# Kernel optimization log

Measured on AMD Instinct MI355X. Metric: run time of the kernel, lower is better.

The kernel has to match this reference:

```python
import jax
import jax.numpy as jnp
import numpy as np
from jax import lax

# Grid / problem dimensions (match init_kwargs / input_specs)
B = 1          # batch_size
D, H, W = 16, 128, 128   # full-resolution voxel grid (z, y, x)
N = 120000     # number of occupied voxels
CIN = 16       # num_input_features
EPS = 1e-5     # MinkowskiBatchNorm eps (eval mode, running stats)


def setup_inputs() -> dict:
    key = jax.random.key(0)
    ks = jax.random.split(key, 24)

    # Unique voxel coordinates (ME.SparseTensor coordinates are unique after quantization)
    perm = jax.random.permutation(ks[0], D * H * W)[:N]
    z = (perm // (H * W)).astype(jnp.int32)
    y = ((perm // W) % H).astype(jnp.int32)
    x = (perm % W).astype(jnp.int32)
    coors = jnp.stack([jnp.zeros(N, jnp.int32), z, y, x], axis=1)  # (batch, z, y, x)

    voxel_features = jax.random.normal(ks[1], (N, CIN), jnp.float32)

    def w(k, shape, fan_in):
        return jax.random.normal(k, shape, jnp.float32) * (1.0 / np.sqrt(fan_in))

    w0 = w(ks[2], (32, 16, 3, 3, 3), 16 * 27)
    w1 = w(ks[3], (32, 32, 3, 3, 3), 32 * 27)
    w2 = w(ks[4], (64, 32, 3, 3, 3), 32 * 27)
    w64 = w(ks[5], (7, 64, 64, 3, 3, 3), 64 * 27)   # the seven 64->64 k=3^3 convs
    w10 = w(ks[6], (64, 64, 3, 1, 1), 64 * 3)        # final k=(3,1,1) conv

    bn32_gamma = 1.0 + 0.1 * jax.random.normal(ks[7], (2, 32), jnp.float32)
    bn32_beta = 0.1 * jax.random.normal(ks[8], (2, 32), jnp.float32)
    bn32_mean = 0.1 * jax.random.normal(ks[9], (2, 32), jnp.float32)
    bn32_var = 0.5 + jax.random.uniform(ks[10], (2, 32), jnp.float32)
    bn64_gamma = 1.0 + 0.1 * jax.random.normal(ks[11], (9, 64), jnp.float32)
    bn64_beta = 0.1 * jax.random.normal(ks[12], (9, 64), jnp.float32)
    bn64_mean = 0.1 * jax.random.normal(ks[13], (9, 64), jnp.float32)
    bn64_var = 0.5 + jax.random.uniform(ks[14], (9, 64), jnp.float32)

    return {
        "voxel_features": voxel_features, "coors": coors,
        "w0": w0, "w1": w1, "w2": w2, "w64": w64, "w10": w10,
        "bn32_gamma": bn32_gamma, "bn32_beta": bn32_beta,
        "bn32_mean": bn32_mean, "bn32_var": bn32_var,
        "bn64_gamma": bn64_gamma, "bn64_beta": bn64_beta,
        "bn64_mean": bn64_mean, "bn64_var": bn64_var,
        "batch_size": B,
    }


def _conv(x, w, stride_z):
    # Minkowski conv with odd kernel is a centered conv; in the z-downsampled
    # dense grid, kernel offsets scaled by tensor stride reduce to ordinary
    # dense conv with 'half' padding per axis and stride on z.
    pads = [(w.shape[2] // 2,) * 2, (w.shape[3] // 2,) * 2, (w.shape[4] // 2,) * 2]
    return lax.conv_general_dilated(
        x, w, (stride_z, 1, 1), pads,
        dimension_numbers=("NCDHW", "OIDHW", "NCDHW"))


def _bn_relu(x, g, b, m, v):
    inv = g / jnp.sqrt(v + EPS)                    # [C]
    sh = (1, -1, 1, 1, 1)
    return jax.nn.relu(x * inv.reshape(sh) + (b - m * inv).reshape(sh))


def _pool_z(occ):
    # strided Minkowski conv output coords = unique(floor(c/2)) of input coords
    return jnp.maximum(occ[:, :, 0::2], occ[:, :, 1::2])


def reference(voxel_features, coors, w0, w1, w2, w64, w10,
              bn32_gamma, bn32_beta, bn32_mean, bn32_var,
              bn64_gamma, bn64_beta, bn64_mean, bn64_var, batch_size):
    b, z, y, x = coors[:, 0], coors[:, 1], coors[:, 2], coors[:, 3]
    # Densify sparse tensor (unoccupied voxels are exact zeros, as in ME)
    h = jnp.zeros((batch_size, D, H, W, CIN), voxel_features.dtype)
    h = h.at[b, z, y, x].set(voxel_features)
    h = jnp.moveaxis(h, -1, 1)                                   # [B,C,D,H,W]
    occ = jnp.zeros((batch_size, 1, D, H, W), voxel_features.dtype)
    occ = occ.at[b, 0, z, y, x].set(1.0)

    # Two 32-channel stride-1 convs: output coords == input coords -> mask with occ
    h = _bn_relu(_conv(h, w0, 1), bn32_gamma[0], bn32_beta[0], bn32_mean[0], bn32_var[0]) * occ
    h = _bn_relu(_conv(h, w1, 1), bn32_gamma[1], bn32_beta[1], bn32_mean[1], bn32_var[1]) * occ

    # 32->64, stride (2,1,1)
    occ = _pool_z(occ)
    h = _bn_relu(_conv(h, w2, 2), bn64_gamma[0], bn64_beta[0], bn64_mean[0], bn64_var[0]) * occ
    # three 64->64 stride-1 convs
    for i in range(3):
        h = _bn_relu(_conv(h, w64[i], 1), bn64_gamma[1 + i], bn64_beta[1 + i], bn64_mean[1 + i], bn64_var[1 + i]) * occ
    # 64->64 stride (2,1,1)
    occ = _pool_z(occ)
    h = _bn_relu(_conv(h, w64[3], 2), bn64_gamma[4], bn64_beta[4], bn64_mean[4], bn64_var[4]) * occ
    # three 64->64 stride-1 convs
    for i in range(3):
        h = _bn_relu(_conv(h, w64[4 + i], 1), bn64_gamma[5 + i], bn64_beta[5 + i], bn64_mean[5 + i], bn64_var[5 + i]) * occ
    # final 64->64, kernel (3,1,1), stride (2,1,1)
    occ = _pool_z(occ)
    h = _bn_relu(_conv(h, w10, 2), bn64_gamma[8], bn64_beta[8], bn64_mean[8], bn64_var[8]) * occ

    # prune is a no-op (all coords in-range by construction); dense() -> [B,C,Dz,H,W]
    n, c, d, hh, ww = h.shape
    return h.reshape(n, c * d, hh, ww)
```

## Files before the change

kernel.cpp:

```cpp
#include <hip/hip_runtime.h>

#define HW 16384

typedef _Float16 half8  __attribute__((ext_vector_type(8)));
typedef _Float16 half4v __attribute__((ext_vector_type(4)));
typedef float    f32x4  __attribute__((ext_vector_type(4)));

typedef __attribute__((address_space(3))) unsigned int lds_u32;
typedef const __attribute__((address_space(1))) unsigned int glb_u32;

__device__ __forceinline__ void gl_lds16(const void* g, void* l) {
    __builtin_amdgcn_global_load_lds((glb_u32*)g, (lds_u32*)l, 16, 0, 0);
}

__global__ void zero4(float4* __restrict__ p, int n4) {
    int i = blockIdx.x * 256 + threadIdx.x;
    if (i < n4) p[i] = make_float4(0.f, 0.f, 0.f, 0.f);
}

__global__ void write_code_f32(float* out, float v) {
    if (threadIdx.x == 0 && blockIdx.x == 0) out[0] = v;
}

__global__ void pack_w(const float* __restrict__ W, _Float16* __restrict__ dst,
                       int CINr, int CINp, int COUT, int KD, int KHW, int NSTEPS) {
    int idx = blockIdx.x * 256 + threadIdx.x;
    int total = (COUT / 16) * NSTEPS * 64;
    if (idx >= total) return;
    int lane = idx & 63;
    int s    = (idx >> 6) % NSTEPS;
    int grp  = idx / (NSTEPS * 64);
    int k0  = s * 32 + (lane >> 4) * 8;
    int t   = k0 / CINp;
    int ci0 = k0 % CINp;
    int co  = grp * 16 + (lane & 15);
    int khw2 = KHW * KHW;
    int dz = t / khw2, r = t % khw2, dy = r / KHW, dx = r % KHW;
    half8 hv;
    for (int j = 0; j < 8; ++j) {
        int ci = ci0 + j;
        float wv = (ci < CINr)
            ? W[(((size_t)co * CINr + ci) * KD + dz) * khw2 + dy * KHW + dx] : 0.0f;
        hv[j] = (_Float16)wv;
    }
    *(half8*)(dst + ((size_t)(grp * NSTEPS + s) * 64 + lane) * 8) = hv;
}

__global__ void scatter_f16(const float* __restrict__ vf, const int* __restrict__ coors,
                            _Float16* __restrict__ act, unsigned char* __restrict__ occ, int n) {
    int i = blockIdx.x * 256 + threadIdx.x;
    if (i >= n) return;
    int z = coors[i * 4 + 1];
    int y = coors[i * 4 + 2];
    int x = coors[i * 4 + 3];
    size_t cell = ((size_t)(z * 130 + (y + 1)) * 130 + (x + 1)) * 40;
    for (int c = 0; c < 16; ++c) act[cell + c] = (_Float16)vf[i * 16 + c];
    occ[z * HW + y * 128 + x] = 1;
}

__global__ void pool_occ(const unsigned char* __restrict__ o0, unsigned char* __restrict__ o1,
                         unsigned char* __restrict__ o2, unsigned char* __restrict__ o3) {
    int p = blockIdx.x * 256 + threadIdx.x;
    if (p >= HW) return;
    unsigned char a[16];
    for (int z = 0; z < 16; ++z) a[z] = o0[z * HW + p];
    for (int z = 0; z < 8; ++z) { a[z] = a[2 * z] | a[2 * z + 1]; o1[z * HW + p] = a[z]; }
    for (int z = 0; z < 4; ++z) { a[z] = a[2 * z] | a[2 * z + 1]; o2[z * HW + p] = a[z]; }
    for (int z = 0; z < 2; ++z) { a[z] = a[2 * z] | a[2 * z + 1]; o3[z * HW + p] = a[z]; }
}

template <int CINp, int COUT, int KD, int KHW, int SZ, int DIN, int DOUT, bool FINAL>
__global__ __launch_bounds__(256, 2)
void conv_mfma(const _Float16* __restrict__ act, const _Float16* __restrict__ apack,
               const float* __restrict__ gm, const float* __restrict__ bt,
               const float* __restrict__ mn, const float* __restrict__ vr,
               const unsigned char* __restrict__ occ, void* __restrict__ outv) {
    constexpr int PADXY  = KHW / 2;
    constexpr int CB     = CINp / 32;
    constexpr int MG     = COUT / 16;
    constexpr int NSTEPS = KD * KHW * KHW * CB;
    constexpr int CS     = CINp + 8;
    constexpr int OCS    = COUT + 8;
    constexpr int NGRAN  = 4 * 130 * CS / 8;
    constexpr int NIT    = (NGRAN + 255) / 256;
    constexpr int OFS    = 1 - PADXY;

    __shared__ _Float16 smem[4 * 130 * CS];

    const int bid = blockIdx.x;
    const int yp = bid & 63;
    const int z0 = bid >> 6;
    const int y0 = yp * 2;
    const int tid  = threadIdx.x;
    const int w    = tid >> 6;
    const int lane = tid & 63;
    const int ylocal = w >> 1;
    const int x0w    = (w & 1) * 64;
    const int n  = lane & 15;
    const int kg = lane >> 4;

    f32x4 acc[MG][4];
    #pragma unroll
    for (int m = 0; m < MG; ++m)
        #pragma unroll
        for (int t = 0; t < 4; ++t) { acc[m][t][0] = 0.f; acc[m][t][1] = 0.f; acc[m][t][2] = 0.f; acc[m][t][3] = 0.f; }

    const int zb = z0 * SZ;
    const int dzlo = (zb == 0) ? 1 : 0;
    const int dzhi = (zb + KD - 1 > DIN) ? (KD - 1) : KD;

    for (int dz = dzlo; dz < dzhi; ++dz) {
        const int zi = zb + dz - 1;
        __syncthreads();
        const _Float16* src = act + (size_t)(zi * 130 + y0) * (130 * CS);
        #pragma unroll
        for (int it = 0; it < NIT; ++it) {
            int g = it * 256 + tid;
            if (g < NGRAN) gl_lds16(src + (size_t)g * 8, smem + (size_t)g * 8);
        }
        asm volatile("s_waitcnt vmcnt(0)" ::: "memory");
        __syncthreads();
        #pragma unroll
        for (int dy = 0; dy < KHW; ++dy) {
            #pragma unroll
            for (int dx = 0; dx < KHW; ++dx) {
                #pragma unroll
                for (int cb = 0; cb < CB; ++cb) {
                    const int sabs = dz * (KHW * KHW * CB) + (dy * KHW + dx) * CB + cb;
                    half8 a[MG];
                    #pragma unroll
                    for (int mg = 0; mg < MG; ++mg)
                        a[mg] = *(const half8*)(apack + ((size_t)(mg * NSTEPS + sabs) * 64 + lane) * 8);
                    const _Float16* bp = smem
                        + ((ylocal + dy + OFS) * 130 + x0w + n + dx + OFS) * CS + cb * 32 + kg * 8;
                    #pragma unroll
                    for (int nt = 0; nt < 4; ++nt) {
                        half8 b = *(const half8*)(bp + nt * 16 * CS);
                        #pragma unroll
                        for (int mg = 0; mg < MG; ++mg)
                            acc[mg][nt] = __builtin_amdgcn_mfma_f32_16x16x32_f16(a[mg], b, acc[mg][nt], 0, 0, 0);
                    }
                }
            }
        }
    }

    const int yo = y0 + ylocal;
    #pragma unroll
    for (int mg = 0; mg < MG; ++mg) {
        const int co0 = mg * 16 + kg * 4;
        const f32x4 gv = *(const f32x4*)(gm + co0);
        const f32x4 bv = *(const f32x4*)(bt + co0);
        const f32x4 mv = *(const f32x4*)(mn + co0);
        const f32x4 vv = *(const f32x4*)(vr + co0);
        float sc[4], sh[4];
        #pragma unroll
        for (int r = 0; r < 4; ++r) {
            sc[r] = gv[r] * __frsqrt_rn(vv[r] + 1e-5f);
            sh[r] = bv[r] - mv[r] * sc[r];
        }
        #pragma unroll
        for (int nt = 0; nt < 4; ++nt) {
            const int x = x0w + nt * 16 + n;
            const float occv = (float)occ[z0 * HW + yo * 128 + x];
            float v0 = fmaxf(fmaf(acc[mg][nt][0], sc[0], sh[0]), 0.f) * occv;
            float v1 = fmaxf(fmaf(acc[mg][nt][1], sc[1], sh[1]), 0.f) * occv;
            float v2 = fmaxf(fmaf(acc[mg][nt][2], sc[2], sh[2]), 0.f) * occv;
            float v3 = fmaxf(fmaf(acc[mg][nt][3], sc[3], sh[3]), 0.f) * occv;
            if constexpr (FINAL) {
                float* o = (float*)outv;
                const int sp = yo * 128 + x;
                o[((size_t)(co0 + 0) * 2 + z0) * HW + sp] = v0;
                o[((size_t)(co0 + 1) * 2 + z0) * HW + sp] = v1;
                o[((size_t)(co0 + 2) * 2 + z0) * HW + sp] = v2;
                o[((size_t)(co0 + 3) * 2 + z0) * HW + sp] = v3;
            } else {
                _Float16* o = (_Float16*)outv;
                half4v hv;
                hv[0] = (_Float16)v0; hv[1] = (_Float16)v1;
                hv[2] = (_Float16)v2; hv[3] = (_Float16)v3;
                *(half4v*)(o + ((size_t)(z0 * 130 + (yo + 1)) * 130 + (x + 1)) * OCS + co0) = hv;
            }
        }
    }
}

extern "C" void kernel_launch(void* const* d_in, const int* in_sizes, int n_in,
                              void* d_out, int out_size, void* d_ws, size_t ws_size,
                              hipStream_t stream) {
    const float* vf    = (const float*)d_in[0];
    const int*   coors = (const int*)d_in[1];
    const float* w0    = (const float*)d_in[2];
    const float* w1    = (const float*)d_in[3];
    const float* w2    = (const float*)d_in[4];
    const float* w64   = (const float*)d_in[5];
    const float* w10   = (const float*)d_in[6];
    const float* g32   = (const float*)d_in[7];
    const float* b32   = (const float*)d_in[8];
    const float* m32   = (const float*)d_in[9];
    const float* v32   = (const float*)d_in[10];
    const float* g64   = (const float*)d_in[11];
    const float* b64   = (const float*)d_in[12];
    const float* m64   = (const float*)d_in[13];
    const float* v64   = (const float*)d_in[14];
    const int N = in_sizes[0] / 16;

    float* out_f = (float*)d_out;

    const size_t R0 = 0;
    const size_t R1 = 21632000;
    const size_t R3 = 43264000;
    const size_t OFF_OCC0 = 62732800;
    const size_t OFF_OCC1 = 62994944;
    const size_t OFF_OCC2 = 63126016;
    const size_t OFF_OCC3 = 63191552;
    const size_t OFF_AP   = 63224320;
    const size_t TOTAL_BYTES = 65018368;
    const size_t S64_8 = 19468800;
    const size_t S64_4 = 9734400;

    if (ws_size < TOTAL_BYTES) {
        write_code_f32<<<dim3(1), dim3(64), 0, stream>>>(out_f, 1.0e8f);
        return;
    }

    char* wsb = (char*)d_ws;
    _Float16* A0p = (_Float16*)(wsb + R0);
    _Float16* A1p = (_Float16*)(wsb + R1);
    _Float16* A3p = (_Float16*)(wsb + R3);
    _Float16* A2p = A1p;
    unsigned char* occ0 = (unsigned char*)(wsb + OFF_OCC0);
    unsigned char* occ1 = (unsigned char*)(wsb + OFF_OCC1);
    unsigned char* occ2 = (unsigned char*)(wsb + OFF_OCC2);
    unsigned char* occ3 = (unsigned char*)(wsb + OFF_OCC3);
    _Float16* AP = (_Float16*)(wsb + OFF_AP);

    const size_t W_A0 = 0, W_A1 = 27648, W_A2 = 55296, W_A3 = 110592, W_A10 = 884736;

    {
        const int n4 = (int)(OFF_OCC1 / 16);
        zero4<<<dim3((n4 + 255) / 256), dim3(256), 0, stream>>>((float4*)wsb, n4);
    }

    auto pk = [&](const float* src, size_t dstoff, int cinr, int cinp, int cout, int kd, int khw) {
        int nsteps = kd * khw * khw * (cinp / 32);
        int total = (cout / 16) * nsteps * 64;
        pack_w<<<dim3((total + 255) / 256), dim3(256), 0, stream>>>(
            src, AP + dstoff, cinr, cinp, cout, kd, khw, nsteps);
    };
    pk(w0, W_A0, 16, 32, 32, 3, 3);
    pk(w1, W_A1, 32, 32, 32, 3, 3);
    pk(w2, W_A2, 32, 32, 64, 3, 3);
    for (int i = 0; i < 7; ++i)
        pk(w64 + (size_t)i * 110592, W_A3 + (size_t)i * 110592, 64, 64, 64, 3, 3);
    pk(w10, W_A10, 64, 64, 64, 3, 1);

    scatter_f16<<<dim3((N + 255) / 256), dim3(256), 0, stream>>>(vf, coors, A0p, occ0, N);
    pool_occ<<<dim3(HW / 256), dim3(256), 0, stream>>>(occ0, occ1, occ2, occ3);

    conv_mfma<32, 32, 3, 3, 1, 16, 16, false><<<dim3(16 * 64), dim3(256), 0, stream>>>(
        A0p, AP + W_A0, g32, b32, m32, v32, occ0, A1p);
    conv_mfma<32, 32, 3, 3, 1, 16, 16, false><<<dim3(16 * 64), dim3(256), 0, stream>>>(
        A1p, AP + W_A1, g32 + 32, b32 + 32, m32 + 32, v32 + 32, occ0, A0p);
    zero4<<<dim3((int)(S64_8 / 16 + 255) / 256, 1, 1), dim3(256), 0, stream>>>((float4*)A2p, (int)(S64_8 / 16));
    conv_mfma<32, 64, 3, 3, 2, 16, 8, false><<<dim3(8 * 64), dim3(256), 0, stream>>>(
        A0p, AP + W_A2, g64, b64, m64, v64, occ1, A2p);
    zero4<<<dim3((int)(S64_4 / 16 + 255) / 256, 1, 1), dim3(256), 0, stream>>>((float4*)A0p, (int)(S64_4 / 16));
    conv_mfma<64, 64, 3, 3, 1, 8, 8, false><<<dim3(8 * 64), dim3(256), 0, stream>>>(
        A2p, AP + W_A3 + 0 * 110592, g64 + 64, b64 + 64, m64 + 64, v64 + 64, occ1, A3p);
    conv_mfma<64, 64, 3, 3, 1, 8, 8, false><<<dim3(8 * 64), dim3(256), 0, stream>>>(
        A3p, AP + W_A3 + 1 * 110592, g64 + 128, b64 + 128, m64 + 128, v64 + 128, occ1, A2p);
    conv_mfma<64, 64, 3, 3, 1, 8, 8, false><<<dim3(8 * 64), dim3(256), 0, stream>>>(
        A2p, AP + W_A3 + 2 * 110592, g64 + 192, b64 + 192, m64 + 192, v64 + 192, occ1, A3p);
    conv_mfma<64, 64, 3, 3, 2, 8, 4, false><<<dim3(4 * 64), dim3(256), 0, stream>>>(
        A3p, AP + W_A3 + 3 * 110592, g64 + 256, b64 + 256, m64 + 256, v64 + 256, occ2, A0p);
    zero4<<<dim3((int)(S64_4 / 16 + 255) / 256, 1, 1), dim3(256), 0, stream>>>((float4*)A1p, (int)(S64_4 / 16));
    conv_mfma<64, 64, 3, 3, 1, 4, 4, false><<<dim3(4 * 64), dim3(256), 0, stream>>>(
        A0p, AP + W_A3 + 4 * 110592, g64 + 320, b64 + 320, m64 + 320, v64 + 320, occ2, A1p);
    conv_mfma<64, 64, 3, 3, 1, 4, 4, false><<<dim3(4 * 64), dim3(256), 0, stream>>>(
        A1p, AP + W_A3 + 5 * 110592, g64 + 384, b64 + 384, m64 + 384, v64 + 384, occ2, A0p);
    conv_mfma<64, 64, 3, 3, 1, 4, 4, false><<<dim3(4 * 64), dim3(256), 0, stream>>>(
        A0p, AP + W_A3 + 6 * 110592, g64 + 448, b64 + 448, m64 + 448, v64 + 448, occ2, A1p);
    conv_mfma<64, 64, 3, 1, 2, 4, 2, true><<<dim3(2 * 64), dim3(256), 0, stream>>>(
        A1p, AP + W_A10, g64 + 512, b64 + 512, m64 + 512, v64 + 512, occ3, out_f);
}
```

Baseline: 370.5 us.

## Zero only padded borders, merge weight packing, and remap workgroups across XCDs

Large full-buffer zero fills of the activation ping-pong buffers are replaced with a border-only zeroing kernel, on the assumption that every conv writes all interior cells. The eleven weight-pack launches become one kernel driven by a descriptor table. The conv kernel also remaps block indices so that consecutive blocks land on strided tiles, aiming for better L2 locality across the chiplets. The risk is correctness if any interior cell or the padding channels are not fully overwritten by the conv that writes them.

```diff
diff --git a/kernel.cpp b/kernel.cpp
--- a/kernel.cpp
+++ b/kernel.cpp
@@ -22,15 +22,47 @@
     if (threadIdx.x == 0 && blockIdx.x == 0) out[0] = v;
 }
 
-__global__ void pack_w(const float* __restrict__ W, _Float16* __restrict__ dst,
-                       int CINr, int CINp, int COUT, int KD, int KHW, int NSTEPS) {
+__global__ void border_zero(_Float16* __restrict__ base, int D, int CS) {
     int idx = blockIdx.x * 256 + threadIdx.x;
-    int total = (COUT / 16) * NSTEPS * 64;
+    int gpc = CS / 8;
+    int total = D * 516 * gpc;
     if (idx >= total) return;
+    int g = idx % gpc;
+    int c = (idx / gpc) % 516;
+    int d = idx / (gpc * 516);
+    int y, x;
+    if (c < 130)      { y = 0;           x = c; }
+    else if (c < 260) { y = 129;         x = c - 130; }
+    else if (c < 388) { y = c - 260 + 1; x = 0; }
+    else              { y = c - 388 + 1; x = 129; }
+    *(float4*)(base + ((size_t)(d * 130 + y) * 130 + x) * CS + g * 8) =
+        make_float4(0.f, 0.f, 0.f, 0.f);
+}
+
+struct PackDesc {
+    const float* src[11];
+    int dstoff[11];
+    int cum[12];
+    int cinr[11];
+    int cinp[11];
+    int cout[11];
+    int khw[11];
+};
+
+__global__ void pack_all(PackDesc pd, _Float16* __restrict__ AP) {
+    int u = blockIdx.x * 256 + threadIdx.x;
+    if (u >= pd.cum[11]) return;
+    int s = 0;
+    while (u >= pd.cum[s + 1]) ++s;
+    int idx = u - pd.cum[s];
+    const int CINr = pd.cinr[s], CINp = pd.cinp[s], KHW = pd.khw[s];
+    const int KD = 3;
+    const int NSTEPS = KD * KHW * KHW * (CINp / 32);
+    const float* W = pd.src[s];
     int lane = idx & 63;
-    int s    = (idx >> 6) % NSTEPS;
+    int st   = (idx >> 6) % NSTEPS;
     int grp  = idx / (NSTEPS * 64);
-    int k0  = s * 32 + (lane >> 4) * 8;
+    int k0  = st * 32 + (lane >> 4) * 8;
     int t   = k0 / CINp;
     int ci0 = k0 % CINp;
     int co  = grp * 16 + (lane & 15);
@@ -43,7 +75,7 @@
             ? W[(((size_t)co * CINr + ci) * KD + dz) * khw2 + dy * KHW + dx] : 0.0f;
         hv[j] = (_Float16)wv;
     }
-    *(half8*)(dst + ((size_t)(grp * NSTEPS + s) * 64 + lane) * 8) = hv;
+    *(half8*)(AP + pd.dstoff[s] + ((size_t)(grp * NSTEPS + st) * 64 + lane) * 8) = hv;
 }
 
 __global__ void scatter_f16(const float* __restrict__ vf, const int* __restrict__ coors,
@@ -84,10 +116,12 @@
     constexpr int NGRAN  = 4 * 130 * CS / 8;
     constexpr int NIT    = (NGRAN + 255) / 256;
     constexpr int OFS    = 1 - PADXY;
+    constexpr int NWG    = DOUT * 64;
 
     __shared__ _Float16 smem[4 * 130 * CS];
 
-    const int bid = blockIdx.x;
+    const int bid0 = blockIdx.x;
+    const int bid = (bid0 & 7) * (NWG / 8) + (bid0 >> 3);
     const int yp = bid & 63;
     const int z0 = bid >> 6;
     const int y0 = yp * 2;
@@ -216,8 +250,6 @@
     const size_t OFF_OCC3 = 63191552;
     const size_t OFF_AP   = 63224320;
     const size_t TOTAL_BYTES = 65018368;
-    const size_t S64_8 = 19468800;
-    const size_t S64_4 = 9734400;
 
     if (ws_size < TOTAL_BYTES) {
         write_code_f32<<<dim3(1), dim3(64), 0, stream>>>(out_f, 1.0e8f);
@@ -237,23 +269,38 @@
 
     const size_t W_A0 = 0, W_A1 = 27648, W_A2 = 55296, W_A3 = 110592, W_A10 = 884736;
 
-    {
-        const int n4 = (int)(OFF_OCC1 / 16);
-        zero4<<<dim3((n4 + 255) / 256), dim3(256), 0, stream>>>((float4*)wsb, n4);
-    }
-
-    auto pk = [&](const float* src, size_t dstoff, int cinr, int cinp, int cout, int kd, int khw) {
-        int nsteps = kd * khw * khw * (cinp / 32);
-        int total = (cout / 16) * nsteps * 64;
-        pack_w<<<dim3((total + 255) / 256), dim3(256), 0, stream>>>(
-            src, AP + dstoff, cinr, cinp, cout, kd, khw, nsteps);
-    };
-    pk(w0, W_A0, 16, 32, 32, 3, 3);
-    pk(w1, W_A1, 32, 32, 32, 3, 3);
-    pk(w2, W_A2, 32, 32, 64, 3, 3);
-    for (int i = 0; i < 7; ++i)
-        pk(w64 + (size_t)i * 110592, W_A3 + (size_t)i * 110592, 64, 64, 64, 3, 3);
-    pk(w10, W_A10, 64, 64, 64, 3, 1);
+    zero4<<<dim3((21632000 / 16 + 255) / 256), dim3(256), 0, stream>>>((float4*)(wsb + R0), 21632000 / 16);
+    zero4<<<dim3((262144 / 16 + 255) / 256), dim3(256), 0, stream>>>((float4*)occ0, 262144 / 16);
+    {
+        int t1 = 16 * 516 * (40 / 8);
+        border_zero<<<dim3((t1 + 255) / 256), dim3(256), 0, stream>>>(A1p, 16, 40);
+        int t3 = 8 * 516 * (72 / 8);
+        border_zero<<<dim3((t3 + 255) / 256), dim3(256), 0, stream>>>(A3p, 8, 72);
+    }
+
+    {
+        PackDesc pd;
+        int units[11] = {3456, 3456, 6912, 13824, 13824, 13824, 13824, 13824, 13824, 13824, 1536};
+        const float* srcs[11] = {w0, w1, w2,
+                                 w64 + 0 * 110592, w64 + 1 * 110592, w64 + 2 * 110592,
+                                 w64 + 3 * 110592, w64 + 4 * 110592, w64 + 5 * 110592,
+                                 w64 + 6 * 110592, w10};
+        int offs[11] = {(int)W_A0, (int)W_A1, (int)W_A2,
+                        (int)(W_A3 + 0 * 110592), (int)(W_A3 + 1 * 110592), (int)(W_A3 + 2 * 110592),
+                        (int)(W_A3 + 3 * 110592), (int)(W_A3 + 4 * 110592), (int)(W_A3 + 5 * 110592),
+                        (int)(W_A3 + 6 * 110592), (int)W_A10};
+        int cinr[11] = {16, 32, 32, 64, 64, 64, 64, 64, 64, 64, 64};
+        int cinp[11] = {32, 32, 32, 64, 64, 64, 64, 64, 64, 64, 64};
+        int cout[11] = {32, 32, 64, 64, 64, 64, 64, 64, 64, 64, 64};
+        int khw[11]  = {3, 3, 3, 3, 3, 3, 3, 3, 3, 3, 1};
+        int c = 0;
+        for (int i = 0; i < 11; ++i) {
+            pd.src[i] = srcs[i]; pd.dstoff[i] = offs[i]; pd.cum[i] = c; c += units[i];
+            pd.cinr[i] = cinr[i]; pd.cinp[i] = cinp[i]; pd.cout[i] = cout[i]; pd.khw[i] = khw[i];
+        }
+        pd.cum[11] = c;
+        pack_all<<<dim3((c + 255) / 256), dim3(256), 0, stream>>>(pd, AP);
+    }
 
     scatter_f16<<<dim3((N + 255) / 256), dim3(256), 0, stream>>>(vf, coors, A0p, occ0, N);
     pool_occ<<<dim3(HW / 256), dim3(256), 0, stream>>>(occ0, occ1, occ2, occ3);
@@ -262,10 +309,16 @@
         A0p, AP + W_A0, g32, b32, m32, v32, occ0, A1p);
     conv_mfma<32, 32, 3, 3, 1, 16, 16, false><<<dim3(16 * 64), dim3(256), 0, stream>>>(
         A1p, AP + W_A1, g32 + 32, b32 + 32, m32 + 32, v32 + 32, occ0, A0p);
-    zero4<<<dim3((int)(S64_8 / 16 + 255) / 256, 1, 1), dim3(256), 0, stream>>>((float4*)A2p, (int)(S64_8 / 16));
+    {
+        int t = 8 * 516 * (72 / 8);
+        border_zero<<<dim3((t + 255) / 256), dim3(256), 0, stream>>>(A2p, 8, 72);
+    }
     conv_mfma<32, 64, 3, 3, 2, 16, 8, false><<<dim3(8 * 64), dim3(256), 0, stream>>>(
         A0p, AP + W_A2, g64, b64, m64, v64, occ1, A2p);
-    zero4<<<dim3((int)(S64_4 / 16 + 255) / 256, 1, 1), dim3(256), 0, stream>>>((float4*)A0p, (int)(S64_4 / 16));
+    {
+        int t = 4 * 516 * (72 / 8);
+        border_zero<<<dim3((t + 255) / 256), dim3(256), 0, stream>>>(A0p, 4, 72);
+    }
     conv_mfma<64, 64, 3, 3, 1, 8, 8, false><<<dim3(8 * 64), dim3(256), 0, stream>>>(
         A2p, AP + W_A3 + 0 * 110592, g64 + 64, b64 + 64, m64 + 64, v64 + 64, occ1, A3p);
     conv_mfma<64, 64, 3, 3, 1, 8, 8, false><<<dim3(8 * 64), dim3(256), 0, stream>>>(
@@ -274,7 +327,10 @@
         A2p, AP + W_A3 + 2 * 110592, g64 + 192, b64 + 192, m64 + 192, v64 + 192, occ1, A3p);
     conv_mfma<64, 64, 3, 3, 2, 8, 4, false><<<dim3(4 * 64), dim3(256), 0, stream>>>(
         A3p, AP + W_A3 + 3 * 110592, g64 + 256, b64 + 256, m64 + 256, v64 + 256, occ2, A0p);
-    zero4<<<dim3((int)(S64_4 / 16 + 255) / 256, 1, 1), dim3(256), 0, stream>>>((float4*)A1p, (int)(S64_4 / 16));
+    {
+        int t = 4 * 516 * (72 / 8);
+        border_zero<<<dim3((t + 255) / 256), dim3(256), 0, stream>>>(A1p, 4, 72);
+    }
     conv_mfma<64, 64, 3, 3, 1, 4, 4, false><<<dim3(4 * 64), dim3(256), 0, stream>>>(
         A0p, AP + W_A3 + 4 * 110592, g64 + 320, b64 + 320, m64 + 320, v64 + 320, occ2, A1p);
     conv_mfma<64, 64, 3, 3, 1, 4, 4, false><<<dim3(4 * 64), dim3(256), 0, stream>>>(
```

Result: faster. 349.8 us (-5.6%).
